# Kernel tuning notes

Hardware: AMD Instinct MI355X
Metric: run time of the kernel (lower is better)

## Reference

```python
import jax, jax.numpy as jnp
import numpy as np
from jax.scipy.special import logsumexp

REG_E = 0.05
N_ITER = 20


def setup_inputs() -> dict:
    key = jax.random.key(0)
    kP, kQ = jax.random.split(key)
    n, m, d = 8192, 8192, 64
    XP = jax.random.normal(kP, (n, d), dtype=jnp.float32)
    XQ = jax.random.normal(kQ, (m, d), dtype=jnp.float32)
    return {"XP": XP, "XQ": XQ}


def sq_cdist(X, Y):
    # squared euclidean distances, (n, m)
    x2 = jnp.sum(X * X, axis=1, keepdims=True)          # (n,1)
    y2 = jnp.sum(Y * Y, axis=1, keepdims=True).T        # (1,m)
    d2 = x2 + y2 - 2.0 * (X @ Y.T)
    return jnp.maximum(d2, 0.0)


def log_sinkhorn(log_a, log_b, C, reg, n_iter):
    # stable log-domain Sinkhorn; returns transport plan exp(M + u[:,None] + v[None,:])
    M = -C / reg                                        # (n,m)
    u0 = jnp.zeros_like(log_a)
    v0 = jnp.zeros_like(log_b)

    def body(carry, _):
        u, v = carry
        u = log_a - logsumexp(M + v[None, :], axis=1)
        v = log_b - logsumexp(M + u[:, None], axis=0)
        return (u, v), None

    (u, v), _ = jax.lax.scan(body, (u0, v0), None, length=n_iter)
    return jnp.exp(M + u[:, None] + v[None, :])


def reference(XP, XQ):
    n, m = XP.shape[0], XQ.shape[0]
    log_uP = jnp.full((n,), -jnp.log(jnp.float32(n)), dtype=XP.dtype)
    log_uQ = jnp.full((m,), -jnp.log(jnp.float32(m)), dtype=XQ.dtype)

    C = sq_cdist(XP, XQ)                                # (n, m)
    Cn = C / jax.lax.stop_gradient(jnp.max(C))
    plan = jax.lax.stop_gradient(
        log_sinkhorn(log_uP, log_uQ, Cn, REG_E, N_ITER)
    )
    return jnp.sum(C * plan)
```

## Files before the change

### kernel.cpp

```cpp
#include <hip/hip_runtime.h>
#include <cmath>

#define NPTS 8192
#define DIM  64
#define LOG2E 1.4426950408889634f
#define LA2   -13.0f

typedef short s16x8  __attribute__((ext_vector_type(8)));
typedef float f32x16 __attribute__((ext_vector_type(16)));

typedef __attribute__((address_space(1))) const unsigned char g8_t;
typedef __attribute__((address_space(3))) unsigned char l8_t;

#if __has_builtin(__builtin_amdgcn_exp2f)
__device__ __forceinline__ float exp2_fast(float x) { return __builtin_amdgcn_exp2f(x); }
#else
__device__ __forceinline__ float exp2_fast(float x) { return exp2f(x); }
#endif
#if __has_builtin(__builtin_amdgcn_logf)
__device__ __forceinline__ float log2_fast(float x) { return __builtin_amdgcn_logf(x); }
#else
__device__ __forceinline__ float log2_fast(float x) { return log2f(x); }
#endif

__device__ __forceinline__ unsigned short f2bf(float x) {
  unsigned u = __float_as_uint(x);
  return (unsigned short)((u + 0x7FFFu + ((u >> 16) & 1u)) >> 16);
}
__device__ __forceinline__ float bf2f(unsigned short b) {
  return __uint_as_float(((unsigned)b) << 16);
}

__global__ __launch_bounds__(256) void prep_kernel(
    const float* __restrict__ XP, const float* __restrict__ XQ,
    unsigned short* __restrict__ Phi, unsigned short* __restrict__ Plo,
    unsigned short* __restrict__ Qhi, unsigned short* __restrict__ Qlo,
    float* __restrict__ x2, float* __restrict__ y2,
    float* __restrict__ scal, float* __restrict__ out) {
  int gid  = blockIdx.x * 256 + threadIdx.x;
  int lane = threadIdx.x & 63;
  int row  = gid >> 6;
  int isP  = row < NPTS;
  int r    = row & (NPTS - 1);
  const float* X = isP ? XP : XQ;
  float x = X[r * DIM + lane];
  unsigned short h = f2bf(x);
  (isP ? Phi : Qhi)[r * DIM + lane] = h;
  (isP ? Plo : Qlo)[r * DIM + lane] = f2bf(x - bf2f(h));
  float s = x * x;
  for (int off = 32; off; off >>= 1) s += __shfl_down(s, off, 64);
  if (lane == 0) (isP ? x2 : y2)[r] = s;
  if (gid == 0) { ((unsigned*)scal)[0] = 0u; out[0] = 0.0f; }
}

template <int MODE, bool FIRST, int MINW>
__global__ __launch_bounds__(256, MINW) void pass_kernel(
    const unsigned short* __restrict__ Ahi, const unsigned short* __restrict__ Alo,
    const unsigned short* __restrict__ Bhi,
    const float* __restrict__ x2row, const float* __restrict__ y2col,
    const float* __restrict__ colPart, const float* __restrict__ rowPart,
    const unsigned* __restrict__ cmaxBits,
    float* __restrict__ outPart, float* __restrict__ outScalar) {
  __shared__ short sB[256 * DIM];
  __shared__ float sCol[512];
  __shared__ float sY2[512];
  __shared__ float sX2[128];
  __shared__ float sU2[128];
  __shared__ float sRed[4];

  const int t  = threadIdx.x;
  const int w  = t >> 6;
  const int l  = t & 63;
  const int g  = l >> 5;
  const int ln = l & 31;
  const int i0 = blockIdx.x * 128;
  const int j0 = blockIdx.y * 512;

  float invC = 0.f, C2L = 0.f;
  if constexpr (MODE != 0) {
    float cmax = __uint_as_float(*cmaxBits);
    invC = 1.0f / (0.05f * cmax);
    C2L  = 2.0f * invC * LOG2E;
  }

  const unsigned char* gB = (const unsigned char*)(Bhi + (size_t)j0 * DIM);
  const unsigned char* gsrc0;
  {
    int s   = w * 512 + l;
    int row = s >> 3;
    int cc  = (s & 7) ^ (row & 7);
    gsrc0 = gB + row * 128 + cc * 16;
  }
  auto stage = [&](int half) {
    const unsigned char* g0 = gsrc0 + half * 32768;
#pragma unroll
    for (int c = 0; c < 8; ++c)
      __builtin_amdgcn_global_load_lds(
          (g8_t*)(g0 + c * 1024),
          (l8_t*)((unsigned char*)sB + w * 8192 + c * 1024), 16, 0, 0);
  };

  s16x8 a_hi[4], a_lo[4];
  {
    const unsigned short* pa = Ahi + (size_t)(i0 + w * 32 + ln) * DIM + g * 8;
#pragma unroll
    for (int ks = 0; ks < 4; ++ks) a_hi[ks] = *(const s16x8*)(pa + ks * 16);
    if constexpr (MODE == 2) {
      const unsigned short* pb = Alo + (size_t)(i0 + w * 32 + ln) * DIM + g * 8;
#pragma unroll
      for (int ks = 0; ks < 4; ++ks) a_lo[ks] = *(const s16x8*)(pb + ks * 16);
    }
  }

  stage(0);

#pragma unroll
  for (int c0 = 0; c0 < 2; ++c0) {
    int c = c0 * 256 + t;
    int j = j0 + c;
    if constexpr (MODE == 0) {
      sY2[c] = y2col[j];
    } else if constexpr (MODE == 1) {
      if constexpr (FIRST) {
        sCol[c] = -invC * y2col[j] * LOG2E;
      } else {
        float s = 0.f;
#pragma unroll
        for (int gy = 0; gy < 16; ++gy) s += colPart[gy * NPTS + j];
        sCol[c] = LA2 - log2_fast(s);
      }
    } else {
      float s = 0.f;
#pragma unroll
      for (int gy = 0; gy < 16; ++gy) s += colPart[gy * NPTS + j];
      sCol[c] = LA2 - log2_fast(s);
      sY2[c] = y2col[j];
    }
  }
  if constexpr (MODE != 1) {
    if (t < 128) {
      sX2[t] = x2row[i0 + t];
      if constexpr (MODE == 2) {
        float s = 0.f;
#pragma unroll
        for (int gy = 0; gy < 16; ++gy) s += rowPart[gy * NPTS + i0 + t];
        sU2[t] = LA2 - log2_fast(s);
      }
    }
  }
  __syncthreads();

  float x2r[16], u2r[16];
  if constexpr (MODE != 1) {
#pragma unroll
    for (int r = 0; r < 16; ++r) {
      int ri = w * 32 + (r & 3) + 8 * (r >> 2) + 4 * g;
      x2r[r] = sX2[ri];
      if constexpr (MODE == 2) u2r[r] = sU2[ri];
    }
  }

  float racc[16];
#pragma unroll
  for (int r = 0; r < 16; ++r) racc[r] = 0.f;
  float accS = 0.f;

  for (int half = 0; half < 2; ++half) {
    if (half) {
      __syncthreads();
      stage(1);
      __syncthreads();
    }
#pragma unroll 2
    for (int ct = 0; ct < 8; ++ct) {
      const int nn = ct * 32 + ln;
      const int n  = half * 256 + nn;
      s16x8 b[4];
#pragma unroll
      for (int ks = 0; ks < 4; ++ks)
        b[ks] = *(const s16x8*)(sB + nn * DIM + (((ks * 2 + g) ^ (ln & 7)) * 8));
      f32x16 acc;
#pragma unroll
      for (int r = 0; r < 16; ++r) acc[r] = 0.f;
#pragma unroll
      for (int ks = 0; ks < 4; ++ks)
        acc = __builtin_amdgcn_mfma_f32_32x32x16_bf16(a_hi[ks], b[ks], acc, 0, 0, 0);

      if constexpr (MODE == 1) {
        float bb = sCol[n];
#pragma unroll
        for (int r = 0; r < 16; ++r)
          racc[r] += exp2_fast(fmaf(C2L, acc[r], bb));
      } else if constexpr (MODE == 0) {
        float y2v = sY2[n];
#pragma unroll
        for (int r = 0; r < 16; ++r)
          accS = fmaxf(accS, fmaf(-2.0f, acc[r], x2r[r] + y2v));
      } else {
        f32x16 acc2;
#pragma unroll
        for (int r = 0; r < 16; ++r) acc2[r] = 0.f;
#pragma unroll
        for (int ks = 0; ks < 4; ++ks)
          acc2 = __builtin_amdgcn_mfma_f32_32x32x16_bf16(a_lo[ks], b[ks], acc2, 0, 0, 0);
        float y2v = sY2[n];
        float bb  = sCol[n];
#pragma unroll
        for (int r = 0; r < 16; ++r) {
          float dot = acc[r] + acc2[r];
          float d2  = fmaxf(fmaf(-2.0f, dot, x2r[r] + y2v), 0.0f);
          accS = fmaf(d2, exp2_fast(fmaf(C2L, dot, u2r[r] + bb)), accS);
        }
      }
    }
  }

  if constexpr (MODE == 1) {
#pragma unroll
    for (int r = 0; r < 16; ++r) {
      float v = racc[r];
      v += __shfl_xor(v, 1, 64);
      v += __shfl_xor(v, 2, 64);
      v += __shfl_xor(v, 4, 64);
      v += __shfl_xor(v, 8, 64);
      v += __shfl_xor(v, 16, 64);
      if (ln == 0)
        outPart[blockIdx.y * NPTS + i0 + w * 32 +
                (r & 3) + 8 * (r >> 2) + 4 * g] = v;
    }
  } else {
    float v = accS;
#pragma unroll
    for (int off = 1; off < 64; off <<= 1) {
      float o = __shfl_xor(v, off, 64);
      v = (MODE == 0) ? fmaxf(v, o) : (v + o);
    }
    if (l == 0) sRed[w] = v;
    __syncthreads();
    if (t == 0) {
      float r0 = (MODE == 0) ? fmaxf(fmaxf(sRed[0], sRed[1]), fmaxf(sRed[2], sRed[3]))
                             : (sRed[0] + sRed[1] + sRed[2] + sRed[3]);
      if constexpr (MODE == 0)
        atomicMax((unsigned*)outScalar, __float_as_uint(r0));
      else
        atomicAdd(outScalar, r0);
    }
  }
}

extern "C" void kernel_launch(void* const* d_in, const int* in_sizes, int n_in,
                              void* d_out, int out_size, void* d_ws, size_t ws_size,
                              hipStream_t stream) {
  (void)in_sizes; (void)n_in; (void)out_size; (void)ws_size;
  const float* XP = (const float*)d_in[0];
  const float* XQ = (const float*)d_in[1];
  float* out = (float*)d_out;

  float* ws    = (float*)d_ws;
  float* x2    = ws;
  float* y2    = ws + 8192;
  float* partU = ws + 16384;
  float* partV = partU + 16 * NPTS;
  float* scal  = partV + 16 * NPTS;
  unsigned short* Phi = (unsigned short*)(scal + 16);
  unsigned short* Plo = Phi + (size_t)NPTS * DIM;
  unsigned short* Qhi = Plo + (size_t)NPTS * DIM;
  unsigned short* Qlo = Qhi + (size_t)NPTS * DIM;

  const unsigned* cmaxB = (const unsigned*)scal;
  dim3 grid(NPTS / 128, NPTS / 512);

  prep_kernel<<<NPTS * 2 * DIM / 256, 256, 0, stream>>>(
      XP, XQ, Phi, Plo, Qhi, Qlo, x2, y2, scal, out);

  pass_kernel<0, false, 4><<<grid, 256, 0, stream>>>(
      Phi, nullptr, Qhi, x2, y2, nullptr, nullptr, cmaxB, nullptr, scal);

  pass_kernel<1, true, 4><<<grid, 256, 0, stream>>>(
      Phi, nullptr, Qhi, nullptr, y2, nullptr, nullptr, cmaxB, partU, nullptr);
  pass_kernel<1, false, 4><<<grid, 256, 0, stream>>>(
      Qhi, nullptr, Phi, nullptr, nullptr, partU, nullptr, cmaxB, partV, nullptr);

  for (int it = 1; it < 20; ++it) {
    pass_kernel<1, false, 4><<<grid, 256, 0, stream>>>(
        Phi, nullptr, Qhi, nullptr, nullptr, partV, nullptr, cmaxB, partU, nullptr);
    pass_kernel<1, false, 4><<<grid, 256, 0, stream>>>(
        Qhi, nullptr, Phi, nullptr, nullptr, partU, nullptr, cmaxB, partV, nullptr);
  }

  pass_kernel<2, false, 2><<<grid, 256, 0, stream>>>(
      Phi, Plo, Qhi, x2, y2, partV, partU, cmaxB, nullptr, out);
}
```

Baseline: 869.6 us.

## Retile Sinkhorn passes to 256x256 blocks with two row slabs per wave

Each Sinkhorn pass block now covers 256 rows by 256 columns instead of 128 by 512. Each wave holds two A row slabs in registers and reuses every B fragment loaded from LDS for both. The whole B tile fits in LDS in one stage, which removes the mid-loop barriers and the second staging step. The cost is twice as many column partials (32 instead of 16) that each consumer must sum, plus more registers per wave for the doubled accumulators.

```diff
diff --git a/kernel.cpp b/kernel.cpp
--- a/kernel.cpp
+++ b/kernel.cpp
@@ -3,6 +3,7 @@
 
 #define NPTS 8192
 #define DIM  64
+#define NPART 32
 #define LOG2E 1.4426950408889634f
 #define LA2   -13.0f
 
@@ -53,7 +54,7 @@
   if (gid == 0) { ((unsigned*)scal)[0] = 0u; out[0] = 0.0f; }
 }
 
-template <int MODE, bool FIRST, int MINW>
+template <int MODE, bool FIRST, int RS, int MINW>
 __global__ __launch_bounds__(256, MINW) void pass_kernel(
     const unsigned short* __restrict__ Ahi, const unsigned short* __restrict__ Alo,
     const unsigned short* __restrict__ Bhi,
@@ -62,8 +63,8 @@
     const unsigned* __restrict__ cmaxBits,
     float* __restrict__ outPart, float* __restrict__ outScalar) {
   __shared__ short sB[256 * DIM];
-  __shared__ float sCol[512];
-  __shared__ float sY2[512];
+  __shared__ float sCol[256];
+  __shared__ float sY2[256];
   __shared__ float sX2[128];
   __shared__ float sU2[128];
   __shared__ float sRed[4];
@@ -73,8 +74,8 @@
   const int l  = t & 63;
   const int g  = l >> 5;
   const int ln = l & 31;
-  const int i0 = blockIdx.x * 128;
-  const int j0 = blockIdx.y * 512;
+  const int i0 = blockIdx.x * 128 * RS;
+  const int j0 = blockIdx.y * 256;
 
   float invC = 0.f, C2L = 0.f;
   if constexpr (MODE != 0) {
@@ -83,58 +84,53 @@
     C2L  = 2.0f * invC * LOG2E;
   }
 
-  const unsigned char* gB = (const unsigned char*)(Bhi + (size_t)j0 * DIM);
-  const unsigned char* gsrc0;
   {
     int s   = w * 512 + l;
     int row = s >> 3;
     int cc  = (s & 7) ^ (row & 7);
-    gsrc0 = gB + row * 128 + cc * 16;
-  }
-  auto stage = [&](int half) {
-    const unsigned char* g0 = gsrc0 + half * 32768;
+    const unsigned char* g0 =
+        (const unsigned char*)(Bhi + (size_t)j0 * DIM) + row * 128 + cc * 16;
 #pragma unroll
     for (int c = 0; c < 8; ++c)
       __builtin_amdgcn_global_load_lds(
           (g8_t*)(g0 + c * 1024),
           (l8_t*)((unsigned char*)sB + w * 8192 + c * 1024), 16, 0, 0);
-  };
-
-  s16x8 a_hi[4], a_lo[4];
+  }
+
+  s16x8 a_hi[RS][4], a_lo[RS][4];
+#pragma unroll
+  for (int s = 0; s < RS; ++s) {
+    const unsigned short* pa =
+        Ahi + (size_t)(i0 + (w * RS + s) * 32 + ln) * DIM + g * 8;
+#pragma unroll
+    for (int ks = 0; ks < 4; ++ks) a_hi[s][ks] = *(const s16x8*)(pa + ks * 16);
+    if constexpr (MODE == 2) {
+      const unsigned short* pb =
+          Alo + (size_t)(i0 + (w * RS + s) * 32 + ln) * DIM + g * 8;
+#pragma unroll
+      for (int ks = 0; ks < 4; ++ks) a_lo[s][ks] = *(const s16x8*)(pb + ks * 16);
+    }
+  }
+
   {
-    const unsigned short* pa = Ahi + (size_t)(i0 + w * 32 + ln) * DIM + g * 8;
-#pragma unroll
-    for (int ks = 0; ks < 4; ++ks) a_hi[ks] = *(const s16x8*)(pa + ks * 16);
-    if constexpr (MODE == 2) {
-      const unsigned short* pb = Alo + (size_t)(i0 + w * 32 + ln) * DIM + g * 8;
-#pragma unroll
-      for (int ks = 0; ks < 4; ++ks) a_lo[ks] = *(const s16x8*)(pb + ks * 16);
-    }
-  }
-
-  stage(0);
-
-#pragma unroll
-  for (int c0 = 0; c0 < 2; ++c0) {
-    int c = c0 * 256 + t;
-    int j = j0 + c;
+    int j = j0 + t;
     if constexpr (MODE == 0) {
-      sY2[c] = y2col[j];
+      sY2[t] = y2col[j];
     } else if constexpr (MODE == 1) {
       if constexpr (FIRST) {
-        sCol[c] = -invC * y2col[j] * LOG2E;
+        sCol[t] = -invC * y2col[j] * LOG2E;
       } else {
         float s = 0.f;
 #pragma unroll
-        for (int gy = 0; gy < 16; ++gy) s += colPart[gy * NPTS + j];
-        sCol[c] = LA2 - log2_fast(s);
+        for (int gy = 0; gy < NPART; ++gy) s += colPart[gy * NPTS + j];
+        sCol[t] = LA2 - log2_fast(s);
       }
     } else {
       float s = 0.f;
 #pragma unroll
-      for (int gy = 0; gy < 16; ++gy) s += colPart[gy * NPTS + j];
-      sCol[c] = LA2 - log2_fast(s);
-      sY2[c] = y2col[j];
+      for (int gy = 0; gy < NPART; ++gy) s += colPart[gy * NPTS + j];
+      sCol[t] = LA2 - log2_fast(s);
+      sY2[t] = y2col[j];
     }
   }
   if constexpr (MODE != 1) {
@@ -143,7 +139,7 @@
       if constexpr (MODE == 2) {
         float s = 0.f;
 #pragma unroll
-        for (int gy = 0; gy < 16; ++gy) s += rowPart[gy * NPTS + i0 + t];
+        for (int gy = 0; gy < NPART; ++gy) s += rowPart[gy * NPTS + i0 + t];
         sU2[t] = LA2 - log2_fast(s);
       }
     }
@@ -160,74 +156,82 @@
     }
   }
 
-  float racc[16];
-#pragma unroll
-  for (int r = 0; r < 16; ++r) racc[r] = 0.f;
+  float racc[RS][16];
+#pragma unroll
+  for (int s = 0; s < RS; ++s)
+#pragma unroll
+    for (int r = 0; r < 16; ++r) racc[s][r] = 0.f;
   float accS = 0.f;
 
-  for (int half = 0; half < 2; ++half) {
-    if (half) {
-      __syncthreads();
-      stage(1);
-      __syncthreads();
-    }
 #pragma unroll 2
-    for (int ct = 0; ct < 8; ++ct) {
-      const int nn = ct * 32 + ln;
-      const int n  = half * 256 + nn;
-      s16x8 b[4];
+  for (int ct = 0; ct < 8; ++ct) {
+    const int n = ct * 32 + ln;
+    s16x8 b[4];
+#pragma unroll
+    for (int ks = 0; ks < 4; ++ks)
+      b[ks] = *(const s16x8*)(sB + n * DIM + (((ks * 2 + g) ^ (ln & 7)) * 8));
+
+    if constexpr (MODE == 1) {
+      float bb = sCol[n];
+#pragma unroll
+      for (int s = 0; s < RS; ++s) {
+        f32x16 acc;
+#pragma unroll
+        for (int r = 0; r < 16; ++r) acc[r] = 0.f;
+#pragma unroll
+        for (int ks = 0; ks < 4; ++ks)
+          acc = __builtin_amdgcn_mfma_f32_32x32x16_bf16(a_hi[s][ks], b[ks], acc, 0, 0, 0);
+#pragma unroll
+        for (int r = 0; r < 16; ++r)
+          racc[s][r] += exp2_fast(fmaf(C2L, acc[r], bb));
+      }
+    } else if constexpr (MODE == 0) {
+      f32x16 acc;
+#pragma unroll
+      for (int r = 0; r < 16; ++r) acc[r] = 0.f;
 #pragma unroll
       for (int ks = 0; ks < 4; ++ks)
-        b[ks] = *(const s16x8*)(sB + nn * DIM + (((ks * 2 + g) ^ (ln & 7)) * 8));
-      f32x16 acc;
-#pragma unroll
-      for (int r = 0; r < 16; ++r) acc[r] = 0.f;
+        acc = __builtin_amdgcn_mfma_f32_32x32x16_bf16(a_hi[0][ks], b[ks], acc, 0, 0, 0);
+      float y2v = sY2[n];
+#pragma unroll
+      for (int r = 0; r < 16; ++r)
+        accS = fmaxf(accS, fmaf(-2.0f, acc[r], x2r[r] + y2v));
+    } else {
+      f32x16 acc, acc2;
+#pragma unroll
+      for (int r = 0; r < 16; ++r) { acc[r] = 0.f; acc2[r] = 0.f; }
 #pragma unroll
       for (int ks = 0; ks < 4; ++ks)
-        acc = __builtin_amdgcn_mfma_f32_32x32x16_bf16(a_hi[ks], b[ks], acc, 0, 0, 0);
-
-      if constexpr (MODE == 1) {
-        float bb = sCol[n];
-#pragma unroll
-        for (int r = 0; r < 16; ++r)
-          racc[r] += exp2_fast(fmaf(C2L, acc[r], bb));
-      } else if constexpr (MODE == 0) {
-        float y2v = sY2[n];
-#pragma unroll
-        for (int r = 0; r < 16; ++r)
-          accS = fmaxf(accS, fmaf(-2.0f, acc[r], x2r[r] + y2v));
-      } else {
-        f32x16 acc2;
-#pragma unroll
-        for (int r = 0; r < 16; ++r) acc2[r] = 0.f;
-#pragma unroll
-        for (int ks = 0; ks < 4; ++ks)
-          acc2 = __builtin_amdgcn_mfma_f32_32x32x16_bf16(a_lo[ks], b[ks], acc2, 0, 0, 0);
-        float y2v = sY2[n];
-        float bb  = sCol[n];
-#pragma unroll
-        for (int r = 0; r < 16; ++r) {
-          float dot = acc[r] + acc2[r];
-          float d2  = fmaxf(fmaf(-2.0f, dot, x2r[r] + y2v), 0.0f);
-          accS = fmaf(d2, exp2_fast(fmaf(C2L, dot, u2r[r] + bb)), accS);
-        }
+        acc = __builtin_amdgcn_mfma_f32_32x32x16_bf16(a_hi[0][ks], b[ks], acc, 0, 0, 0);
+#pragma unroll
+      for (int ks = 0; ks < 4; ++ks)
+        acc2 = __builtin_amdgcn_mfma_f32_32x32x16_bf16(a_lo[0][ks], b[ks], acc2, 0, 0, 0);
+      float y2v = sY2[n];
+      float bb  = sCol[n];
+#pragma unroll
+      for (int r = 0; r < 16; ++r) {
+        float dot = acc[r] + acc2[r];
+        float d2  = fmaxf(fmaf(-2.0f, dot, x2r[r] + y2v), 0.0f);
+        accS = fmaf(d2, exp2_fast(fmaf(C2L, dot, u2r[r] + bb)), accS);
       }
     }
   }
 
   if constexpr (MODE == 1) {
 #pragma unroll
-    for (int r = 0; r < 16; ++r) {
-      float v = racc[r];
-      v += __shfl_xor(v, 1, 64);
-      v += __shfl_xor(v, 2, 64);
-      v += __shfl_xor(v, 4, 64);
-      v += __shfl_xor(v, 8, 64);
-      v += __shfl_xor(v, 16, 64);
-      if (ln == 0)
-        outPart[blockIdx.y * NPTS + i0 + w * 32 +
-                (r & 3) + 8 * (r >> 2) + 4 * g] = v;
-    }
+    for (int s = 0; s < RS; ++s)
+#pragma unroll
+      for (int r = 0; r < 16; ++r) {
+        float v = racc[s][r];
+        v += __shfl_xor(v, 1, 64);
+        v += __shfl_xor(v, 2, 64);
+        v += __shfl_xor(v, 4, 64);
+        v += __shfl_xor(v, 8, 64);
+        v += __shfl_xor(v, 16, 64);
+        if (ln == 0)
+          outPart[blockIdx.y * NPTS + i0 + (w * RS + s) * 32 +
+                  (r & 3) + 8 * (r >> 2) + 4 * g] = v;
+      }
   } else {
     float v = accS;
 #pragma unroll
@@ -260,34 +264,35 @@
   float* x2    = ws;
   float* y2    = ws + 8192;
   float* partU = ws + 16384;
-  float* partV = partU + 16 * NPTS;
-  float* scal  = partV + 16 * NPTS;
+  float* partV = partU + NPART * NPTS;
+  float* scal  = partV + NPART * NPTS;
   unsigned short* Phi = (unsigned short*)(scal + 16);
   unsigned short* Plo = Phi + (size_t)NPTS * DIM;
   unsigned short* Qhi = Plo + (size_t)NPTS * DIM;
   unsigned short* Qlo = Qhi + (size_t)NPTS * DIM;
 
   const unsigned* cmaxB = (const unsigned*)scal;
-  dim3 grid(NPTS / 128, NPTS / 512);
+  dim3 gridH(NPTS / 256, NPTS / 256);
+  dim3 gridW(NPTS / 128, NPTS / 256);
 
   prep_kernel<<<NPTS * 2 * DIM / 256, 256, 0, stream>>>(
       XP, XQ, Phi, Plo, Qhi, Qlo, x2, y2, scal, out);
 
-  pass_kernel<0, false, 4><<<grid, 256, 0, stream>>>(
+  pass_kernel<0, false, 1, 4><<<gridW, 256, 0, stream>>>(
       Phi, nullptr, Qhi, x2, y2, nullptr, nullptr, cmaxB, nullptr, scal);
 
-  pass_kernel<1, true, 4><<<grid, 256, 0, stream>>>(
+  pass_kernel<1, true, 2, 4><<<gridH, 256, 0, stream>>>(
       Phi, nullptr, Qhi, nullptr, y2, nullptr, nullptr, cmaxB, partU, nullptr);
-  pass_kernel<1, false, 4><<<grid, 256, 0, stream>>>(
+  pass_kernel<1, false, 2, 4><<<gridH, 256, 0, stream>>>(
       Qhi, nullptr, Phi, nullptr, nullptr, partU, nullptr, cmaxB, partV, nullptr);
 
   for (int it = 1; it < 20; ++it) {
-    pass_kernel<1, false, 4><<<grid, 256, 0, stream>>>(
+    pass_kernel<1, false, 2, 4><<<gridH, 256, 0, stream>>>(
         Phi, nullptr, Qhi, nullptr, nullptr, partV, nullptr, cmaxB, partU, nullptr);
-    pass_kernel<1, false, 4><<<grid, 256, 0, stream>>>(
+    pass_kernel<1, false, 2, 4><<<gridH, 256, 0, stream>>>(
         Qhi, nullptr, Phi, nullptr, nullptr, partU, nullptr, cmaxB, partV, nullptr);
   }
 
-  pass_kernel<2, false, 2><<<grid, 256, 0, stream>>>(
+  pass_kernel<2, false, 1, 2><<<gridW, 256, 0, stream>>>(
       Phi, Plo, Qhi, x2, y2, partV, partU, cmaxB, nullptr, out);
 }
```

New measurement: 1.011 ms. +16.2%, slower.

## Use dedicated small-tile Sinkhorn kernel with atomic row sums and triple-buffered accumulators

Applied to the files above, without the earlier changes.

Replaces the 40 Sinkhorn half-iteration launches with a new sink_kernel that uses 128x128 tiles, 16x16x32 bf16 MFMA, direct global-to-LDS loads and occupancy 8. Row sums are accumulated with atomicAdd into a rotating set of three buffers: one is read, one is written, and the third is zeroed for the next pass. This removes the 16-way partial-sum array and the per-column 16-load reduction. The intent is higher occupancy and less partial-sum traffic per pass, at the cost of more blocks, more atomics and float atomic nondeterminism.

```diff
diff --git a/kernel.cpp b/kernel.cpp
--- a/kernel.cpp
+++ b/kernel.cpp
@@ -7,6 +7,7 @@
 #define LA2   -13.0f
 
 typedef short s16x8  __attribute__((ext_vector_type(8)));
+typedef float f32x4  __attribute__((ext_vector_type(4)));
 typedef float f32x16 __attribute__((ext_vector_type(16)));
 
 typedef __attribute__((address_space(1))) const unsigned char g8_t;
@@ -36,7 +37,7 @@
     unsigned short* __restrict__ Phi, unsigned short* __restrict__ Plo,
     unsigned short* __restrict__ Qhi, unsigned short* __restrict__ Qlo,
     float* __restrict__ x2, float* __restrict__ y2,
-    float* __restrict__ scal, float* __restrict__ out) {
+    float* __restrict__ rs0, float* __restrict__ scal, float* __restrict__ out) {
   int gid  = blockIdx.x * 256 + threadIdx.x;
   int lane = threadIdx.x & 63;
   int row  = gid >> 6;
@@ -50,17 +51,104 @@
   float s = x * x;
   for (int off = 32; off; off >>= 1) s += __shfl_down(s, off, 64);
   if (lane == 0) (isP ? x2 : y2)[r] = s;
+  if (gid < NPTS) rs0[gid] = 0.0f;
   if (gid == 0) { ((unsigned*)scal)[0] = 0u; out[0] = 0.0f; }
 }
 
-template <int MODE, bool FIRST, int MINW>
+template <bool FIRST>
+__global__ __launch_bounds__(256, 8) void sink_kernel(
+    const unsigned short* __restrict__ Ahi, const unsigned short* __restrict__ Bhi,
+    const float* __restrict__ y2col, const float* __restrict__ rsRead,
+    float* __restrict__ rsWrite, float* __restrict__ rsZero,
+    const unsigned* __restrict__ cmaxBits) {
+  __shared__ short sB[128 * DIM];
+  __shared__ float sCol[128];
+
+  const int t   = threadIdx.x;
+  const int w   = t >> 6;
+  const int l   = t & 63;
+  const int q   = l >> 4;
+  const int c16 = l & 15;
+  const int i0  = blockIdx.x * 128;
+  const int j0  = blockIdx.y * 128;
+
+  if (t < 2) rsZero[(blockIdx.y * 64 + blockIdx.x) * 2 + t] = 0.0f;
+
+  const float cmax = __uint_as_float(*cmaxBits);
+  const float invC = 1.0f / (0.05f * cmax);
+  const float C2L  = 2.0f * invC * LOG2E;
+
+  {
+    int ss  = w * 256 + l;
+    int row = ss >> 3;
+    int lc  = (ss & 7) ^ (row & 7);
+    const unsigned char* g0 =
+        (const unsigned char*)(Bhi + (size_t)j0 * DIM) + row * 128 + lc * 16;
+#pragma unroll
+    for (int c = 0; c < 4; ++c)
+      __builtin_amdgcn_global_load_lds(
+          (g8_t*)(g0 + c * 1024),
+          (l8_t*)((unsigned char*)sB + w * 4096 + c * 1024), 16, 0, 0);
+  }
+
+  s16x8 a[2][2];
+#pragma unroll
+  for (int rg = 0; rg < 2; ++rg) {
+    const unsigned short* pa =
+        Ahi + (size_t)(i0 + w * 32 + rg * 16 + c16) * DIM + q * 8;
+    a[rg][0] = *(const s16x8*)(pa);
+    a[rg][1] = *(const s16x8*)(pa + 32);
+  }
+
+  if (t < 128) {
+    int j = j0 + t;
+    sCol[t] = FIRST ? (-invC * y2col[j] * LOG2E)
+                    : (LA2 - log2_fast(rsRead[j]));
+  }
+  __syncthreads();
+
+  f32x4 racc[2];
+  racc[0] = f32x4{0.f, 0.f, 0.f, 0.f};
+  racc[1] = f32x4{0.f, 0.f, 0.f, 0.f};
+
+#pragma unroll
+  for (int cg = 0; cg < 8; ++cg) {
+    const int n = cg * 16 + c16;
+    s16x8 b0 = *(const s16x8*)(sB + n * DIM + ((q ^ (n & 7)) * 8));
+    s16x8 b1 = *(const s16x8*)(sB + n * DIM + (((q + 4) ^ (n & 7)) * 8));
+    float bb = sCol[n];
+#pragma unroll
+    for (int rg = 0; rg < 2; ++rg) {
+      f32x4 acc = f32x4{0.f, 0.f, 0.f, 0.f};
+      acc = __builtin_amdgcn_mfma_f32_16x16x32_bf16(a[rg][0], b0, acc, 0, 0, 0);
+      acc = __builtin_amdgcn_mfma_f32_16x16x32_bf16(a[rg][1], b1, acc, 0, 0, 0);
+#pragma unroll
+      for (int r = 0; r < 4; ++r)
+        racc[rg][r] += exp2_fast(fmaf(C2L, acc[r], bb));
+    }
+  }
+
+#pragma unroll
+  for (int rg = 0; rg < 2; ++rg)
+#pragma unroll
+    for (int r = 0; r < 4; ++r) {
+      float v = racc[rg][r];
+      v += __shfl_xor(v, 1, 64);
+      v += __shfl_xor(v, 2, 64);
+      v += __shfl_xor(v, 4, 64);
+      v += __shfl_xor(v, 8, 64);
+      if (c16 == 0)
+        atomicAdd(&rsWrite[i0 + w * 32 + rg * 16 + q * 4 + r], v);
+    }
+}
+
+template <int MODE, int MINW>
 __global__ __launch_bounds__(256, MINW) void pass_kernel(
     const unsigned short* __restrict__ Ahi, const unsigned short* __restrict__ Alo,
     const unsigned short* __restrict__ Bhi,
     const float* __restrict__ x2row, const float* __restrict__ y2col,
-    const float* __restrict__ colPart, const float* __restrict__ rowPart,
-    const unsigned* __restrict__ cmaxBits,
-    float* __restrict__ outPart, float* __restrict__ outScalar) {
+    const float* __restrict__ vRS, const float* __restrict__ uRS,
+    const unsigned* __restrict__ cmaxBits, float* __restrict__ outScalar) {
   __shared__ short sB[256 * DIM];
   __shared__ float sCol[512];
   __shared__ float sY2[512];
@@ -120,49 +208,25 @@
     int j = j0 + c;
     if constexpr (MODE == 0) {
       sY2[c] = y2col[j];
-    } else if constexpr (MODE == 1) {
-      if constexpr (FIRST) {
-        sCol[c] = -invC * y2col[j] * LOG2E;
-      } else {
-        float s = 0.f;
-#pragma unroll
-        for (int gy = 0; gy < 16; ++gy) s += colPart[gy * NPTS + j];
-        sCol[c] = LA2 - log2_fast(s);
-      }
     } else {
-      float s = 0.f;
-#pragma unroll
-      for (int gy = 0; gy < 16; ++gy) s += colPart[gy * NPTS + j];
-      sCol[c] = LA2 - log2_fast(s);
+      sCol[c] = LA2 - log2_fast(vRS[j]);
       sY2[c] = y2col[j];
     }
   }
-  if constexpr (MODE != 1) {
-    if (t < 128) {
-      sX2[t] = x2row[i0 + t];
-      if constexpr (MODE == 2) {
-        float s = 0.f;
-#pragma unroll
-        for (int gy = 0; gy < 16; ++gy) s += rowPart[gy * NPTS + i0 + t];
-        sU2[t] = LA2 - log2_fast(s);
-      }
-    }
+  if (t < 128) {
+    sX2[t] = x2row[i0 + t];
+    if constexpr (MODE == 2) sU2[t] = LA2 - log2_fast(uRS[i0 + t]);
   }
   __syncthreads();
 
   float x2r[16], u2r[16];
-  if constexpr (MODE != 1) {
-#pragma unroll
-    for (int r = 0; r < 16; ++r) {
-      int ri = w * 32 + (r & 3) + 8 * (r >> 2) + 4 * g;
-      x2r[r] = sX2[ri];
-      if constexpr (MODE == 2) u2r[r] = sU2[ri];
-    }
-  }
-
-  float racc[16];
-#pragma unroll
-  for (int r = 0; r < 16; ++r) racc[r] = 0.f;
+#pragma unroll
+  for (int r = 0; r < 16; ++r) {
+    int ri = w * 32 + (r & 3) + 8 * (r >> 2) + 4 * g;
+    x2r[r] = sX2[ri];
+    if constexpr (MODE == 2) u2r[r] = sU2[ri];
+  }
+
   float accS = 0.f;
 
   for (int half = 0; half < 2; ++half) {
@@ -185,13 +249,7 @@
 #pragma unroll
       for (int ks = 0; ks < 4; ++ks)
         acc = __builtin_amdgcn_mfma_f32_32x32x16_bf16(a_hi[ks], b[ks], acc, 0, 0, 0);
-
-      if constexpr (MODE == 1) {
-        float bb = sCol[n];
-#pragma unroll
-        for (int r = 0; r < 16; ++r)
-          racc[r] += exp2_fast(fmaf(C2L, acc[r], bb));
-      } else if constexpr (MODE == 0) {
+      if constexpr (MODE == 0) {
         float y2v = sY2[n];
 #pragma unroll
         for (int r = 0; r < 16; ++r)
@@ -215,36 +273,21 @@
     }
   }
 
-  if constexpr (MODE == 1) {
-#pragma unroll
-    for (int r = 0; r < 16; ++r) {
-      float v = racc[r];
-      v += __shfl_xor(v, 1, 64);
-      v += __shfl_xor(v, 2, 64);
-      v += __shfl_xor(v, 4, 64);
-      v += __shfl_xor(v, 8, 64);
-      v += __shfl_xor(v, 16, 64);
-      if (ln == 0)
-        outPart[blockIdx.y * NPTS + i0 + w * 32 +
-                (r & 3) + 8 * (r >> 2) + 4 * g] = v;
-    }
-  } else {
-    float v = accS;
-#pragma unroll
-    for (int off = 1; off < 64; off <<= 1) {
-      float o = __shfl_xor(v, off, 64);
-      v = (MODE == 0) ? fmaxf(v, o) : (v + o);
-    }
-    if (l == 0) sRed[w] = v;
-    __syncthreads();
-    if (t == 0) {
-      float r0 = (MODE == 0) ? fmaxf(fmaxf(sRed[0], sRed[1]), fmaxf(sRed[2], sRed[3]))
-                             : (sRed[0] + sRed[1] + sRed[2] + sRed[3]);
-      if constexpr (MODE == 0)
-        atomicMax((unsigned*)outScalar, __float_as_uint(r0));
-      else
-        atomicAdd(outScalar, r0);
-    }
+  float v = accS;
+#pragma unroll
+  for (int off = 1; off < 64; off <<= 1) {
+    float o = __shfl_xor(v, off, 64);
+    v = (MODE == 0) ? fmaxf(v, o) : (v + o);
+  }
+  if (l == 0) sRed[w] = v;
+  __syncthreads();
+  if (t == 0) {
+    float r0 = (MODE == 0) ? fmaxf(fmaxf(sRed[0], sRed[1]), fmaxf(sRed[2], sRed[3]))
+                           : (sRed[0] + sRed[1] + sRed[2] + sRed[3]);
+    if constexpr (MODE == 0)
+      atomicMax((unsigned*)outScalar, __float_as_uint(r0));
+    else
+      atomicAdd(outScalar, r0);
   }
 }
 
@@ -256,38 +299,40 @@
   const float* XQ = (const float*)d_in[1];
   float* out = (float*)d_out;
 
-  float* ws    = (float*)d_ws;
-  float* x2    = ws;
-  float* y2    = ws + 8192;
-  float* partU = ws + 16384;
-  float* partV = partU + 16 * NPTS;
-  float* scal  = partV + 16 * NPTS;
+  float* ws   = (float*)d_ws;
+  float* x2   = ws;
+  float* y2   = ws + 8192;
+  float* rs0  = ws + 16384;
+  float* rs1  = ws + 24576;
+  float* rs2  = ws + 32768;
+  float* scal = ws + 40960;
   unsigned short* Phi = (unsigned short*)(scal + 16);
   unsigned short* Plo = Phi + (size_t)NPTS * DIM;
   unsigned short* Qhi = Plo + (size_t)NPTS * DIM;
   unsigned short* Qlo = Qhi + (size_t)NPTS * DIM;
+  float* rs[3] = {rs0, rs1, rs2};
 
   const unsigned* cmaxB = (const unsigned*)scal;
-  dim3 grid(NPTS / 128, NPTS / 512);
+  dim3 gridS(NPTS / 128, NPTS / 128);
+  dim3 gridW(NPTS / 128, NPTS / 512);
 
   prep_kernel<<<NPTS * 2 * DIM / 256, 256, 0, stream>>>(
-      XP, XQ, Phi, Plo, Qhi, Qlo, x2, y2, scal, out);
-
-  pass_kernel<0, false, 4><<<grid, 256, 0, stream>>>(
-      Phi, nullptr, Qhi, x2, y2, nullptr, nullptr, cmaxB, nullptr, scal);
-
-  pass_kernel<1, true, 4><<<grid, 256, 0, stream>>>(
-      Phi, nullptr, Qhi, nullptr, y2, nullptr, nullptr, cmaxB, partU, nullptr);
-  pass_kernel<1, false, 4><<<grid, 256, 0, stream>>>(
-      Qhi, nullptr, Phi, nullptr, nullptr, partU, nullptr, cmaxB, partV, nullptr);
-
-  for (int it = 1; it < 20; ++it) {
-    pass_kernel<1, false, 4><<<grid, 256, 0, stream>>>(
-        Phi, nullptr, Qhi, nullptr, nullptr, partV, nullptr, cmaxB, partU, nullptr);
-    pass_kernel<1, false, 4><<<grid, 256, 0, stream>>>(
-        Qhi, nullptr, Phi, nullptr, nullptr, partU, nullptr, cmaxB, partV, nullptr);
-  }
-
-  pass_kernel<2, false, 2><<<grid, 256, 0, stream>>>(
-      Phi, Plo, Qhi, x2, y2, partV, partU, cmaxB, nullptr, out);
-}
+      XP, XQ, Phi, Plo, Qhi, Qlo, x2, y2, rs0, scal, out);
+
+  pass_kernel<0, 4><<<gridW, 256, 0, stream>>>(
+      Phi, nullptr, Qhi, x2, y2, nullptr, nullptr, cmaxB, scal);
+
+  for (int p = 0; p < 40; ++p) {
+    const unsigned short* A = (p & 1) ? Qhi : Phi;
+    const unsigned short* B = (p & 1) ? Phi : Qhi;
+    if (p == 0)
+      sink_kernel<true><<<gridS, 256, 0, stream>>>(
+          A, B, y2, nullptr, rs[0], rs[1], cmaxB);
+    else
+      sink_kernel<false><<<gridS, 256, 0, stream>>>(
+          A, B, nullptr, rs[(p + 2) % 3], rs[p % 3], rs[(p + 1) % 3], cmaxB);
+  }
+
+  pass_kernel<2, 2><<<gridW, 256, 0, stream>>>(
+      Phi, Plo, Qhi, x2, y2, rs[0], rs[2], cmaxB, out);
+}
```

After: 2.430 ms. +179.4%, slower.
